# Kernel tuning notes

Hardware: AMD Instinct MI355X
Metric: run time of the kernel (lower is better)

The kernel has to match this reference:

```python
import jax, jax.numpy as jnp
import numpy as np

N, D = 8192, 64


def setup_inputs() -> dict:
    key = jax.random.key(0)
    k1, k2, k3 = jax.random.split(key, 3)
    X = jax.random.normal(k1, (N, D), dtype=jnp.float32)
    target = jax.random.normal(k2, (N,), dtype=jnp.float32)
    params = jax.random.uniform(k3, (D,), dtype=jnp.float32)  # positive ARD weights
    return {"X": X, "target": target, "params": params}


def reference(X, target, params):
    # ARD-RBF kernel: k(x, y) = exp(-sum(params * (x - y)^2))
    # = exp(-||xs - ys||^2) with xs = x * sqrt(params)
    Xs = X * jnp.sqrt(params)  # [N, D]
    sq = jnp.sum(Xs * Xs, axis=-1)  # [N]
    d2 = jnp.maximum(sq[:, None] + sq[None, :] - 2.0 * (Xs @ Xs.T), 0.0)  # [N, N]
    K = jnp.exp(-d2)
    # torch version initializes K = eye(N) and never overwrites the diagonal
    n = X.shape[0]
    K = K.at[jnp.arange(n), jnp.arange(n)].set(1.0)
    K_target = jnp.outer(target, target)  # [N, N]
    kta = jnp.sum(K * K_target) / (n * jnp.sqrt(jnp.sum(K * K)))
    return -kta
```

## Files before the change

kernel.cpp:

```cpp
#include <hip/hip_runtime.h>
#include <hip/hip_bf16.h>

#define NROWS 8192
#define DIM 64
#define NT 64
#define NTRI (NT * (NT + 1) / 2)

typedef __attribute__((ext_vector_type(8))) short short8;
typedef __attribute__((ext_vector_type(4))) float f32x4;

static constexpr float LOG2E = 1.4426950408889634f;

#if defined(__has_builtin) && __has_builtin(__builtin_amdgcn_exp2f)
#define EXP2F(x) __builtin_amdgcn_exp2f(x)
#else
#define EXP2F(x) exp2f(x)
#endif

__global__ __launch_bounds__(256) void prep_kernel(const float* __restrict__ X,
                                                   const float* __restrict__ params,
                                                   float* __restrict__ Lsq,
                                                   short* __restrict__ Xp) {
    int tid  = threadIdx.x;
    int wave = tid >> 6, lane = tid & 63;
    int r8 = lane >> 3, c = lane & 7;
    int row = blockIdx.x * 32 + wave * 8 + r8;

    const float* xr = X + row * DIM + c * 8;
    float4 x0 = *(const float4*)xr;
    float4 x1 = *(const float4*)(xr + 4);
    float4 p0 = *(const float4*)(params + c * 8);
    float4 p1 = *(const float4*)(params + c * 8 + 4);

    float v[8];
    v[0] = x0.x * sqrtf(p0.x); v[1] = x0.y * sqrtf(p0.y);
    v[2] = x0.z * sqrtf(p0.z); v[3] = x0.w * sqrtf(p0.w);
    v[4] = x1.x * sqrtf(p1.x); v[5] = x1.y * sqrtf(p1.y);
    v[6] = x1.z * sqrtf(p1.z); v[7] = x1.w * sqrtf(p1.w);

    short8 h;
    float s = 0.f;
    #pragma unroll
    for (int i = 0; i < 8; ++i) {
        __hip_bfloat16 b = __float2bfloat16(v[i]);
        union { __hip_bfloat16 bb; short ss; } u; u.bb = b;
        h[i] = u.ss;
        float bf = __bfloat162float(b);
        s += bf * bf;
    }

    int panel = row >> 4, pr = row & 15;
    ((short8*)Xp)[panel * 128 + c * 16 + pr] = h;

    #pragma unroll
    for (int m = 1; m < 8; m <<= 1) s += __shfl_xor(s, m, 64);
    if (c == 0) Lsq[row] = LOG2E * s;
}

__global__ __launch_bounds__(256, 2) void kta_main(const short* __restrict__ Xp,
                                                   const float* __restrict__ Lsq,
                                                   const float* __restrict__ t,
                                                   float2* __restrict__ partial) {
    int k = blockIdx.x;
    int it = (int)((129.0f - sqrtf(16641.0f - 8.0f * (float)k)) * 0.5f);
    if (it > NT - 1) it = NT - 1;
    while ((it * (129 - it)) / 2 > k) --it;
    while (((it + 1) * (128 - it)) / 2 <= k) ++it;
    int jt = it + (k - (it * (129 - it)) / 2);

    int tid  = threadIdx.x;
    int wave = tid >> 6, lane = tid & 63;
    int quad = lane >> 4, l16 = lane & 15;
    int rbase = it * 128 + (wave >> 1) * 64;
    int cbase = jt * 128 + (wave & 1) * 64;

    const short8* Xpv = (const short8*)Xp;
    int pA0 = rbase >> 4, pB0 = cbase >> 4;
    short8 afr[4][2], bfr[4][2];
    #pragma unroll
    for (int rt = 0; rt < 4; ++rt) {
        #pragma unroll
        for (int kc = 0; kc < 2; ++kc) {
            afr[rt][kc] = Xpv[(pA0 + rt) * 128 + (kc * 4 + quad) * 16 + l16];
            bfr[rt][kc] = Xpv[(pB0 + rt) * 128 + (kc * 4 + quad) * 16 + l16];
        }
    }

    float LsqR[4][4], tR[4][4];
    #pragma unroll
    for (int rt = 0; rt < 4; ++rt)
        #pragma unroll
        for (int r = 0; r < 4; ++r) {
            int row = rbase + rt * 16 + quad * 4 + r;
            LsqR[rt][r] = Lsq[row];
            tR[rt][r]   = t[row];
        }
    float LsqC[4], tC[4];
    #pragma unroll
    for (int ct = 0; ct < 4; ++ct) {
        int col = cbase + ct * 16 + l16;
        LsqC[ct] = Lsq[col];
        tC[ct]   = t[col];
    }

    f32x4 c[4][4];
    #pragma unroll
    for (int rt = 0; rt < 4; ++rt)
        #pragma unroll
        for (int ct = 0; ct < 4; ++ct)
            c[rt][ct] = (f32x4){0.f, 0.f, 0.f, 0.f};

    #pragma unroll
    for (int rt = 0; rt < 4; ++rt)
        #pragma unroll
        for (int ct = 0; ct < 4; ++ct) {
            c[rt][ct] = __builtin_amdgcn_mfma_f32_16x16x32_bf16(afr[rt][0], bfr[ct][0], c[rt][ct], 0, 0, 0);
            c[rt][ct] = __builtin_amdgcn_mfma_f32_16x16x32_bf16(afr[rt][1], bfr[ct][1], c[rt][ct], 0, 0, 0);
        }

    bool diagwave = (it == jt) && ((wave >> 1) == (wave & 1));

    float s1 = 0.f, s2a = 0.f, s2b = 0.f;

    auto run = [&](int DIAG) {
        #pragma unroll
        for (int rt = 0; rt < 4; ++rt) {
            #pragma unroll
            for (int r = 0; r < 4; ++r) {
                float nr = LsqR[rt][r];
                float s1row = 0.f;
                #pragma unroll
                for (int ct = 0; ct < 4; ++ct) {
                    float dot = c[rt][ct][r];
                    float K = EXP2F(fmaf(dot, 2.0f * LOG2E, -(nr + LsqC[ct])));
                    if (DIAG && (rt == ct) && ((quad * 4 + r) == l16))
                        K = 1.0f;
                    s1row = fmaf(K, tC[ct], s1row);
                    if (ct & 2) s2b = fmaf(K, K, s2b);
                    else        s2a = fmaf(K, K, s2a);
                }
                s1 = fmaf(s1row, tR[rt][r], s1);
            }
        }
    };
    if (diagwave) run(1); else run(0);

    float s2 = s2a + s2b;
    float w = (it == jt) ? 1.0f : 2.0f;
    s1 *= w; s2 *= w;
    #pragma unroll
    for (int m = 32; m > 0; m >>= 1) {
        s1 += __shfl_xor(s1, m, 64);
        s2 += __shfl_xor(s2, m, 64);
    }

    __shared__ float2 red[4];
    if (lane == 0) red[wave] = make_float2(s1, s2);
    __syncthreads();
    if (tid == 0) {
        float2 a = red[0], b = red[1], cc = red[2], d = red[3];
        partial[k] = make_float2(a.x + b.x + cc.x + d.x, a.y + b.y + cc.y + d.y);
    }
}

__global__ __launch_bounds__(256) void finalize_kernel(const float2* __restrict__ partial,
                                                       float* __restrict__ out) {
    float s1 = 0.f, s2 = 0.f;
    for (int i = threadIdx.x; i < NTRI; i += 256) {
        float2 p = partial[i];
        s1 += p.x;
        s2 += p.y;
    }
    #pragma unroll
    for (int m = 32; m > 0; m >>= 1) {
        s1 += __shfl_xor(s1, m, 64);
        s2 += __shfl_xor(s2, m, 64);
    }
    __shared__ float r1[4], r2[4];
    int wave = threadIdx.x >> 6, lane = threadIdx.x & 63;
    if (lane == 0) { r1[wave] = s1; r2[wave] = s2; }
    __syncthreads();
    if (threadIdx.x == 0) {
        float a = r1[0] + r1[1] + r1[2] + r1[3];
        float b = r2[0] + r2[1] + r2[2] + r2[3];
        out[0] = -a / ((float)NROWS * sqrtf(b));
    }
}

extern "C" void kernel_launch(void* const* d_in, const int* in_sizes, int n_in,
                              void* d_out, int out_size, void* d_ws, size_t ws_size,
                              hipStream_t stream) {
    const float* X      = (const float*)d_in[0];
    const float* target = (const float*)d_in[1];
    const float* params = (const float*)d_in[2];
    float* out = (float*)d_out;

    float* ws = (float*)d_ws;
    float2* partial = (float2*)ws;
    float* Lsq = ws + 8192;
    short* Xp  = (short*)(ws + 16384);

    prep_kernel<<<NROWS / 32, 256, 0, stream>>>(X, params, Lsq, Xp);
    kta_main<<<NTRI, 256, 0, stream>>>(Xp, Lsq, target, partial);
    finalize_kernel<<<1, 256, 0, stream>>>(partial, out);
}
```

Measured before the change: 74.74 us.

## Process two triangular tiles per block with prefetch of second tile's B fragments

Each block now handles two consecutive upper-triangular 128x128 tiles instead of one, which halves the grid size. When the second tile shares the same row-tile, its B fragments and column norms are loaded before the first tile's exp epilogue runs, so those loads can overlap the epilogue, and the A fragments and row data are reused. Where the pair crosses a row boundary, A and B are reloaded after the first epilogue. The cost is higher register pressure and a longer serial path per block. NTRI (2080) is even, so the pairing covers every tile, and the finalize kernel sums the smaller partial array.

```diff
diff --git a/kernel.cpp b/kernel.cpp
--- a/kernel.cpp
+++ b/kernel.cpp
@@ -5,6 +5,8 @@
 #define DIM 64
 #define NT 64
 #define NTRI (NT * (NT + 1) / 2)
+#define TPB 2
+#define NBLK (NTRI / TPB)
 
 typedef __attribute__((ext_vector_type(8))) short short8;
 typedef __attribute__((ext_vector_type(4))) float f32x4;
@@ -61,32 +63,34 @@
                                                    const float* __restrict__ Lsq,
                                                    const float* __restrict__ t,
                                                    float2* __restrict__ partial) {
-    int k = blockIdx.x;
-    int it = (int)((129.0f - sqrtf(16641.0f - 8.0f * (float)k)) * 0.5f);
+    int k0 = blockIdx.x * TPB;
+    int it = (int)((129.0f - sqrtf(16641.0f - 8.0f * (float)k0)) * 0.5f);
     if (it > NT - 1) it = NT - 1;
-    while ((it * (129 - it)) / 2 > k) --it;
-    while (((it + 1) * (128 - it)) / 2 <= k) ++it;
-    int jt = it + (k - (it * (129 - it)) / 2);
+    while ((it * (129 - it)) / 2 > k0) --it;
+    while (((it + 1) * (128 - it)) / 2 <= k0) ++it;
+    int jt = it + (k0 - (it * (129 - it)) / 2);
 
     int tid  = threadIdx.x;
     int wave = tid >> 6, lane = tid & 63;
     int quad = lane >> 4, l16 = lane & 15;
-    int rbase = it * 128 + (wave >> 1) * 64;
-    int cbase = jt * 128 + (wave & 1) * 64;
+    int wr = (wave >> 1) * 64, wc = (wave & 1) * 64;
 
     const short8* Xpv = (const short8*)Xp;
+
+    short8 afr[4][2], bfr[4][2];
+    float LsqR[4][4], tR[4][4];
+    float LsqC0[4], tC0[4], LsqC1[4], tC1[4];
+
+    int rbase = it * 128 + wr;
+    int cbase = jt * 128 + wc;
     int pA0 = rbase >> 4, pB0 = cbase >> 4;
-    short8 afr[4][2], bfr[4][2];
-    #pragma unroll
-    for (int rt = 0; rt < 4; ++rt) {
+    #pragma unroll
+    for (int rt = 0; rt < 4; ++rt)
         #pragma unroll
         for (int kc = 0; kc < 2; ++kc) {
             afr[rt][kc] = Xpv[(pA0 + rt) * 128 + (kc * 4 + quad) * 16 + l16];
             bfr[rt][kc] = Xpv[(pB0 + rt) * 128 + (kc * 4 + quad) * 16 + l16];
         }
-    }
-
-    float LsqR[4][4], tR[4][4];
     #pragma unroll
     for (int rt = 0; rt < 4; ++rt)
         #pragma unroll
@@ -95,59 +99,117 @@
             LsqR[rt][r] = Lsq[row];
             tR[rt][r]   = t[row];
         }
-    float LsqC[4], tC[4];
     #pragma unroll
     for (int ct = 0; ct < 4; ++ct) {
         int col = cbase + ct * 16 + l16;
-        LsqC[ct] = Lsq[col];
-        tC[ct]   = t[col];
+        LsqC0[ct] = Lsq[col];
+        tC0[ct]   = t[col];
     }
 
     f32x4 c[4][4];
-    #pragma unroll
-    for (int rt = 0; rt < 4; ++rt)
-        #pragma unroll
-        for (int ct = 0; ct < 4; ++ct)
+
+    #pragma unroll
+    for (int rt = 0; rt < 4; ++rt)
+        #pragma unroll
+        for (int ct = 0; ct < 4; ++ct) {
             c[rt][ct] = (f32x4){0.f, 0.f, 0.f, 0.f};
-
-    #pragma unroll
-    for (int rt = 0; rt < 4; ++rt)
-        #pragma unroll
-        for (int ct = 0; ct < 4; ++ct) {
             c[rt][ct] = __builtin_amdgcn_mfma_f32_16x16x32_bf16(afr[rt][0], bfr[ct][0], c[rt][ct], 0, 0, 0);
             c[rt][ct] = __builtin_amdgcn_mfma_f32_16x16x32_bf16(afr[rt][1], bfr[ct][1], c[rt][ct], 0, 0, 0);
         }
 
-    bool diagwave = (it == jt) && ((wave >> 1) == (wave & 1));
+    int it1 = it, jt1 = jt + 1;
+    bool rowcross = (jt1 == NT);
+    if (rowcross) { it1 = it + 1; jt1 = it1; }
+    int cbase1 = jt1 * 128 + wc;
+    int pB1 = cbase1 >> 4;
+
+    if (!rowcross) {
+        #pragma unroll
+        for (int rt = 0; rt < 4; ++rt)
+            #pragma unroll
+            for (int kc = 0; kc < 2; ++kc)
+                bfr[rt][kc] = Xpv[(pB1 + rt) * 128 + (kc * 4 + quad) * 16 + l16];
+        #pragma unroll
+        for (int ct = 0; ct < 4; ++ct) {
+            int col = cbase1 + ct * 16 + l16;
+            LsqC1[ct] = Lsq[col];
+            tC1[ct]   = t[col];
+        }
+    }
 
     float s1 = 0.f, s2a = 0.f, s2b = 0.f;
 
-    auto run = [&](int DIAG) {
-        #pragma unroll
-        for (int rt = 0; rt < 4; ++rt) {
+    auto epi = [&](const float (&LC)[4], const float (&TC)[4], bool dwave, float w) {
+        float t1 = 0.f, t2a = 0.f, t2b = 0.f;
+        auto body = [&](int DIAG) {
+            #pragma unroll
+            for (int rt = 0; rt < 4; ++rt) {
+                #pragma unroll
+                for (int r = 0; r < 4; ++r) {
+                    float nr = LsqR[rt][r];
+                    float s1row = 0.f;
+                    #pragma unroll
+                    for (int ct = 0; ct < 4; ++ct) {
+                        float dot = c[rt][ct][r];
+                        float K = EXP2F(fmaf(dot, 2.0f * LOG2E, -(nr + LC[ct])));
+                        if (DIAG && (rt == ct) && ((quad * 4 + r) == l16))
+                            K = 1.0f;
+                        s1row = fmaf(K, TC[ct], s1row);
+                        if (ct & 2) t2b = fmaf(K, K, t2b);
+                        else        t2a = fmaf(K, K, t2a);
+                    }
+                    t1 = fmaf(s1row, tR[rt][r], t1);
+                }
+            }
+        };
+        if (dwave) body(1); else body(0);
+        s1  = fmaf(t1,  w, s1);
+        s2a = fmaf(t2a, w, s2a);
+        s2b = fmaf(t2b, w, s2b);
+    };
+
+    bool dw0 = (it == jt) && ((wave >> 1) == (wave & 1));
+    epi(LsqC0, tC0, dw0, (it == jt) ? 1.0f : 2.0f);
+
+    if (rowcross) {
+        int rbase1 = it1 * 128 + wr;
+        int pA1 = rbase1 >> 4;
+        #pragma unroll
+        for (int rt = 0; rt < 4; ++rt)
+            #pragma unroll
+            for (int kc = 0; kc < 2; ++kc) {
+                afr[rt][kc] = Xpv[(pA1 + rt) * 128 + (kc * 4 + quad) * 16 + l16];
+                bfr[rt][kc] = Xpv[(pB1 + rt) * 128 + (kc * 4 + quad) * 16 + l16];
+            }
+        #pragma unroll
+        for (int rt = 0; rt < 4; ++rt)
             #pragma unroll
             for (int r = 0; r < 4; ++r) {
-                float nr = LsqR[rt][r];
-                float s1row = 0.f;
-                #pragma unroll
-                for (int ct = 0; ct < 4; ++ct) {
-                    float dot = c[rt][ct][r];
-                    float K = EXP2F(fmaf(dot, 2.0f * LOG2E, -(nr + LsqC[ct])));
-                    if (DIAG && (rt == ct) && ((quad * 4 + r) == l16))
-                        K = 1.0f;
-                    s1row = fmaf(K, tC[ct], s1row);
-                    if (ct & 2) s2b = fmaf(K, K, s2b);
-                    else        s2a = fmaf(K, K, s2a);
-                }
-                s1 = fmaf(s1row, tR[rt][r], s1);
+                int row = rbase1 + rt * 16 + quad * 4 + r;
+                LsqR[rt][r] = Lsq[row];
+                tR[rt][r]   = t[row];
             }
-        }
-    };
-    if (diagwave) run(1); else run(0);
+        #pragma unroll
+        for (int ct = 0; ct < 4; ++ct) {
+            int col = cbase1 + ct * 16 + l16;
+            LsqC1[ct] = Lsq[col];
+            tC1[ct]   = t[col];
+        }
+    }
+
+    #pragma unroll
+    for (int rt = 0; rt < 4; ++rt)
+        #pragma unroll
+        for (int ct = 0; ct < 4; ++ct) {
+            c[rt][ct] = (f32x4){0.f, 0.f, 0.f, 0.f};
+            c[rt][ct] = __builtin_amdgcn_mfma_f32_16x16x32_bf16(afr[rt][0], bfr[ct][0], c[rt][ct], 0, 0, 0);
+            c[rt][ct] = __builtin_amdgcn_mfma_f32_16x16x32_bf16(afr[rt][1], bfr[ct][1], c[rt][ct], 0, 0, 0);
+        }
+
+    bool dw1 = rowcross && ((wave >> 1) == (wave & 1));
+    epi(LsqC1, tC1, dw1, rowcross ? 1.0f : 2.0f);
 
     float s2 = s2a + s2b;
-    float w = (it == jt) ? 1.0f : 2.0f;
-    s1 *= w; s2 *= w;
     #pragma unroll
     for (int m = 32; m > 0; m >>= 1) {
         s1 += __shfl_xor(s1, m, 64);
@@ -159,14 +221,14 @@
     __syncthreads();
     if (tid == 0) {
         float2 a = red[0], b = red[1], cc = red[2], d = red[3];
-        partial[k] = make_float2(a.x + b.x + cc.x + d.x, a.y + b.y + cc.y + d.y);
+        partial[blockIdx.x] = make_float2(a.x + b.x + cc.x + d.x, a.y + b.y + cc.y + d.y);
     }
 }
 
 __global__ __launch_bounds__(256) void finalize_kernel(const float2* __restrict__ partial,
                                                        float* __restrict__ out) {
     float s1 = 0.f, s2 = 0.f;
-    for (int i = threadIdx.x; i < NTRI; i += 256) {
+    for (int i = threadIdx.x; i < NBLK; i += 256) {
         float2 p = partial[i];
         s1 += p.x;
         s2 += p.y;
@@ -201,6 +263,6 @@
     short* Xp  = (short*)(ws + 16384);
 
     prep_kernel<<<NROWS / 32, 256, 0, stream>>>(X, params, Lsq, Xp);
-    kta_main<<<NTRI, 256, 0, stream>>>(Xp, Lsq, target, partial);
+    kta_main<<<NBLK, 256, 0, stream>>>(Xp, Lsq, target, partial);
     finalize_kernel<<<1, 256, 0, stream>>>(partial, out);
 }
```

Result: no change. 75.41 us (+0.9%).

## Stage A/B panels in LDS and interleave MFMA with exp epilogue per row tile

Applied to the files above, without the earlier changes.

Each block now cooperatively copies its 128-row A and B panels into shared memory, so waves no longer issue duplicate global fragment loads. The MFMA for each row tile is computed just before its exp/reduction epilogue, keeping only four accumulators live instead of sixteen. Occupancy is raised from 2 to 3 blocks per SIMD through launch bounds. The cost is a __syncthreads, 32 KB of LDS per block that may cap occupancy, and extra LDS reads.

```diff
diff --git a/kernel.cpp b/kernel.cpp
--- a/kernel.cpp
+++ b/kernel.cpp
@@ -57,7 +57,7 @@
     if (c == 0) Lsq[row] = LOG2E * s;
 }
 
-__global__ __launch_bounds__(256, 2) void kta_main(const short* __restrict__ Xp,
+__global__ __launch_bounds__(256, 3) void kta_main(const short* __restrict__ Xp,
                                                    const float* __restrict__ Lsq,
                                                    const float* __restrict__ t,
                                                    float2* __restrict__ partial) {
@@ -71,20 +71,22 @@
     int tid  = threadIdx.x;
     int wave = tid >> 6, lane = tid & 63;
     int quad = lane >> 4, l16 = lane & 15;
+
+    __shared__ short8 As[1024];
+    __shared__ short8 Bs[1024];
+
+    const short8* Xpv  = (const short8*)Xp;
+    const short8* Asrc = Xpv + (size_t)it * 1024;
+    const short8* Bsrc = Xpv + (size_t)jt * 1024;
+
+    #pragma unroll
+    for (int i = 0; i < 4; ++i) {
+        As[tid + i * 256] = Asrc[tid + i * 256];
+        Bs[tid + i * 256] = Bsrc[tid + i * 256];
+    }
+
     int rbase = it * 128 + (wave >> 1) * 64;
     int cbase = jt * 128 + (wave & 1) * 64;
-
-    const short8* Xpv = (const short8*)Xp;
-    int pA0 = rbase >> 4, pB0 = cbase >> 4;
-    short8 afr[4][2], bfr[4][2];
-    #pragma unroll
-    for (int rt = 0; rt < 4; ++rt) {
-        #pragma unroll
-        for (int kc = 0; kc < 2; ++kc) {
-            afr[rt][kc] = Xpv[(pA0 + rt) * 128 + (kc * 4 + quad) * 16 + l16];
-            bfr[rt][kc] = Xpv[(pB0 + rt) * 128 + (kc * 4 + quad) * 16 + l16];
-        }
-    }
 
     float LsqR[4][4], tR[4][4];
     #pragma unroll
@@ -103,35 +105,40 @@
         tC[ct]   = t[col];
     }
 
-    f32x4 c[4][4];
-    #pragma unroll
-    for (int rt = 0; rt < 4; ++rt)
+    __syncthreads();
+
+    int lpA = (wave >> 1) * 4;
+    int lpB = (wave & 1) * 4;
+
+    short8 bfr[4][2];
+    #pragma unroll
+    for (int ct = 0; ct < 4; ++ct)
         #pragma unroll
-        for (int ct = 0; ct < 4; ++ct)
-            c[rt][ct] = (f32x4){0.f, 0.f, 0.f, 0.f};
-
-    #pragma unroll
-    for (int rt = 0; rt < 4; ++rt)
-        #pragma unroll
-        for (int ct = 0; ct < 4; ++ct) {
-            c[rt][ct] = __builtin_amdgcn_mfma_f32_16x16x32_bf16(afr[rt][0], bfr[ct][0], c[rt][ct], 0, 0, 0);
-            c[rt][ct] = __builtin_amdgcn_mfma_f32_16x16x32_bf16(afr[rt][1], bfr[ct][1], c[rt][ct], 0, 0, 0);
-        }
+        for (int kc = 0; kc < 2; ++kc)
+            bfr[ct][kc] = Bs[(lpB + ct) * 128 + (kc * 4 + quad) * 16 + l16];
 
     bool diagwave = (it == jt) && ((wave >> 1) == (wave & 1));
-
     float s1 = 0.f, s2a = 0.f, s2b = 0.f;
 
-    auto run = [&](int DIAG) {
+    auto body = [&](int DIAG) {
         #pragma unroll
         for (int rt = 0; rt < 4; ++rt) {
+            short8 a0 = As[(lpA + rt) * 128 + quad * 16 + l16];
+            short8 a1 = As[(lpA + rt) * 128 + (4 + quad) * 16 + l16];
+            f32x4 cc[4];
+            #pragma unroll
+            for (int ct = 0; ct < 4; ++ct) {
+                cc[ct] = (f32x4){0.f, 0.f, 0.f, 0.f};
+                cc[ct] = __builtin_amdgcn_mfma_f32_16x16x32_bf16(a0, bfr[ct][0], cc[ct], 0, 0, 0);
+                cc[ct] = __builtin_amdgcn_mfma_f32_16x16x32_bf16(a1, bfr[ct][1], cc[ct], 0, 0, 0);
+            }
             #pragma unroll
             for (int r = 0; r < 4; ++r) {
                 float nr = LsqR[rt][r];
                 float s1row = 0.f;
                 #pragma unroll
                 for (int ct = 0; ct < 4; ++ct) {
-                    float dot = c[rt][ct][r];
+                    float dot = cc[ct][r];
                     float K = EXP2F(fmaf(dot, 2.0f * LOG2E, -(nr + LsqC[ct])));
                     if (DIAG && (rt == ct) && ((quad * 4 + r) == l16))
                         K = 1.0f;
@@ -143,7 +150,7 @@
             }
         }
     };
-    if (diagwave) run(1); else run(0);
+    if (diagwave) body(1); else body(0);
 
     float s2 = s2a + s2b;
     float w = (it == jt) ? 1.0f : 2.0f;
```

After: 74.88 us. About the same (+0.2%).
